# Kernel optimization log

Hardware: AMD Instinct MI355X
Metric: run time of the kernel (lower is better)

The kernel has to match this reference:

```python
import jax, jax.numpy as jnp
import numpy as np

HEADS = 4
DIM_HEAD = 64
MAP_SIZE = 16
SCALE = DIM_HEAD ** (-0.5)


def _split_heads(x):
    # torch rearrange 'b (dim_head heads) h w -> b heads (h w) dim_head'
    B, C, H, W = x.shape
    x = x.reshape(B, DIM_HEAD, HEADS, H * W)
    return jnp.transpose(x, (0, 2, 3, 1))  # [B, heads, N, dim_head]


def _merge_heads(x, H, W):
    # torch rearrange 'b heads (h w) dim_head -> b (dim_head heads) h w'
    B, h, N, d = x.shape
    return jnp.transpose(x, (0, 3, 1, 2)).reshape(B, d * h, H, W)


def setup_inputs() -> dict:
    key = jax.random.key(0)
    ks = jax.random.split(key, 6)
    feat = jax.random.normal(ks[0], (4, 256, 96, 96), jnp.float32)
    semantic_map = jax.random.normal(ks[1], (4, 256, 16, 16), jnp.float32)
    # 1x1 conv weights, shape [out_ch, in_ch]; scaled like fan-in init
    W_feat_qv = 0.05 * jax.random.normal(ks[2], (512, 256), jnp.float32)
    W_map_qv = 0.05 * jax.random.normal(ks[3], (512, 256), jnp.float32)
    W_feat_out = 0.05 * jax.random.normal(ks[4], (256, 256), jnp.float32)
    W_map_out = 0.05 * jax.random.normal(ks[5], (256, 256), jnp.float32)
    return {
        "feat": feat,
        "semantic_map": semantic_map,
        "W_feat_qv": W_feat_qv,
        "W_map_qv": W_map_qv,
        "W_feat_out": W_feat_out,
        "W_map_out": W_map_out,
    }


def reference(feat, semantic_map, W_feat_qv, W_map_qv, W_feat_out, W_map_out):
    B, C, H, W = feat.shape
    # 1x1 convs == per-pixel channel matmuls
    fqv = jnp.einsum("oc,bchw->bohw", W_feat_qv, feat)
    feat_q, feat_v = jnp.split(fqv, 2, axis=1)
    mqv = jnp.einsum("oc,bchw->bohw", W_map_qv, semantic_map)
    map_q, map_v = jnp.split(mqv, 2, axis=1)

    feat_q, feat_v = _split_heads(feat_q), _split_heads(feat_v)  # [B,h,N,d]
    map_q, map_v = _split_heads(map_q), _split_heads(map_v)      # [B,h,M,d]

    attn = jnp.einsum("bhid,bhjd->bhij", feat_q, map_q) * SCALE  # [B,h,N,M]
    feat_map_attn = jax.nn.softmax(attn, axis=-1)  # normalize over map tokens j
    map_feat_attn = jax.nn.softmax(attn, axis=-2)  # normalize over feat tokens i

    feat_o = jnp.einsum("bhij,bhjd->bhid", feat_map_attn, map_v)   # [B,h,N,d]
    map_o = jnp.einsum("bhji,bhjd->bhid", map_feat_attn, feat_v)   # [B,h,M,d]

    feat_o = _merge_heads(feat_o, H, W)
    map_o = _merge_heads(map_o, MAP_SIZE, MAP_SIZE)

    feat_out = jnp.einsum("oc,bchw->bohw", W_feat_out, feat_o)
    map_out = jnp.einsum("oc,bchw->bohw", W_map_out, map_o)
    return feat_out, map_out
```

## Files before the change

### kernel.cpp

```cpp
#include <hip/hip_runtime.h>
#include <stdint.h>

#define DI static __device__ __forceinline__

constexpr int NTOK = 9216;
constexpr float ATT_SCALE = 0.125f;

typedef short bf16x8 __attribute__((ext_vector_type(8)));
typedef float f32x4  __attribute__((ext_vector_type(4)));

DI f32x4 mfma16(bf16x8 a, bf16x8 b, f32x4 c) {
  return __builtin_amdgcn_mfma_f32_16x16x32_bf16(a, b, c, 0, 0, 0);
}

DI float lo2f(uint32_t u) { union { uint32_t i; float f; } v; v.i = u << 16; return v.f; }
DI float hi2f(uint32_t u) { union { uint32_t i; float f; } v; v.i = u & 0xffff0000u; return v.f; }
DI float b2f(uint16_t u) { union { uint32_t i; float f; } v; v.i = ((uint32_t)u) << 16; return v.f; }
DI uint16_t f2b(float f) {
  union { float f; uint32_t i; } v; v.f = f;
  uint32_t r = (v.i + 0x7fffu + ((v.i >> 16) & 1u)) >> 16;
  return (uint16_t)r;
}

template<int DT> DI float ld1(const void* p, size_t off) {
  if constexpr (DT) return b2f(((const uint16_t*)p)[off]);
  else              return ((const float*)p)[off];
}
template<int DT> DI void st1(void* p, size_t off, float v) {
  if constexpr (DT) ((uint16_t*)p)[off] = f2b(v);
  else              ((float*)p)[off] = v;
}
template<int DT> DI void load8(const void* p, size_t off, float* o) {
  if constexpr (DT) {
    const uint4 w = *(const uint4*)((const uint16_t*)p + off);
    o[0] = lo2f(w.x); o[1] = hi2f(w.x); o[2] = lo2f(w.y); o[3] = hi2f(w.y);
    o[4] = lo2f(w.z); o[5] = hi2f(w.z); o[6] = lo2f(w.w); o[7] = hi2f(w.w);
  } else {
    const float4 a = *(const float4*)((const float*)p + off);
    const float4 b = *(const float4*)((const float*)p + off + 4);
    o[0] = a.x; o[1] = a.y; o[2] = a.z; o[3] = a.w;
    o[4] = b.x; o[5] = b.y; o[6] = b.z; o[7] = b.w;
  }
}

__global__ void detect_dtype(const uint32_t* __restrict__ w, int* __restrict__ flag) {
  const int l = threadIdx.x;
  int cl = 0;
  #pragma unroll
  for (int i = 0; i < 4; ++i) {
    const float b = b2f((uint16_t)(w[l + i * 64] & 0xffffu));
    const float ab = fabsf(b);
    cl += (ab > 1e-4f && ab < 0.5f) ? 1 : 0;
  }
  cl += __shfl_xor(cl, 1);  cl += __shfl_xor(cl, 2);  cl += __shfl_xor(cl, 4);
  cl += __shfl_xor(cl, 8);  cl += __shfl_xor(cl, 16); cl += __shfl_xor(cl, 32);
  if (l == 0) flag[0] = (cl >= 128) ? 1 : 0;
}

template<int DT>
DI void prep_w_body(const void* __restrict__ Wfqv, const void* __restrict__ Wfo,
                    uint16_t* __restrict__ WqvP, uint16_t* __restrict__ WfoP)
{
  const int r = blockIdx.x, c = threadIdx.x;
  if (r < 512) {
    const int sel = r >> 8, within = r & 255;
    const int h = within >> 6, d = within & 63;
    const int src = sel * 256 + d * 4 + h;
    const int q = (c >> 3) & 3, j = c & 7;
    const int kp = (c & ~31) | (q << 3) | ((j + 2 * q) & 7);
    WqvP[(size_t)r * 256 + c] = f2b(ld1<DT>(Wfqv, (size_t)src * 256 + kp));
  } else {
    const int ro = r - 512;
    WfoP[(size_t)ro * 256 + c] =
        f2b(ld1<DT>(Wfo, (size_t)ro * 256 + (c & 63) * 4 + (c >> 6)));
  }
}
__global__ __launch_bounds__(256) void prep_w(
    const void* Wfqv, const void* Wfo, uint16_t* WqvP, uint16_t* WfoP,
    const int* __restrict__ flag)
{
  if (flag[0]) prep_w_body<1>(Wfqv, Wfo, WqvP, WfoP);
  else         prep_w_body<0>(Wfqv, Wfo, WqvP, WfoP);
}

constexpr int PB = 264;

template<int DT>
DI void gemm0_body(uint16_t* Bsh, const uint16_t* __restrict__ WqvP,
                   const void* __restrict__ X,
                   uint16_t* __restrict__ FQ, uint16_t* __restrict__ FVt)
{
  const int tid = threadIdx.x;
  const int w = tid >> 6, lane = tid & 63;
  const int l = lane & 15, quad = lane >> 4;
  const int n0 = blockIdx.x * 256;
  const int hh = blockIdx.y;
  const int bb = blockIdx.z;
  const size_t bh = (size_t)bb * 4 + hh;

  f32x4 acc[8][4];
  #pragma unroll
  for (int a = 0; a < 8; ++a)
    #pragma unroll
    for (int b = 0; b < 4; ++b) { acc[a][b].x = 0.f; acc[a][b].y = 0.f; acc[a][b].z = 0.f; acc[a][b].w = 0.f; }

  const int cst = tid >> 3;
  const int nst = (tid & 7) * 32;

  for (int ks = 0; ks < 8; ++ks) {
    {
      const size_t gbase = ((size_t)bb * 256 + ks * 32 + cst) * NTOK + n0 + nst;
      #pragma unroll
      for (int q = 0; q < 4; ++q) {
        if constexpr (DT) {
          *(uint4*)(Bsh + cst * PB + nst + q * 8) =
              *(const uint4*)((const uint16_t*)X + gbase + q * 8);
        } else {
          float xv[8];
          load8<0>(X, gbase + q * 8, xv);
          uint16_t pk[8];
          #pragma unroll
          for (int j = 0; j < 8; ++j) pk[j] = f2b(xv[j]);
          *(uint4*)(Bsh + cst * PB + nst + q * 8) = *(const uint4*)pk;
        }
      }
    }
    __syncthreads();
    bf16x8 af[8];
    #pragma unroll
    for (int mt = 0; mt < 8; ++mt) {
      const int arow = (mt >> 2) * 256 + hh * 64 + (mt & 3) * 16 + l;
      af[mt] = *(const bf16x8*)(WqvP + (size_t)arow * 256 + ks * 32 + quad * 8);
    }
    #pragma unroll
    for (int nt = 0; nt < 4; ++nt) {
      const int nl = w * 64 + nt * 16 + l;
      union { uint16_t h[8]; bf16x8 v; } bu;
      #pragma unroll
      for (int j = 0; j < 8; ++j)
        bu.h[j] = Bsh[(quad * 8 + ((j + 2 * quad) & 7)) * PB + nl];
      #pragma unroll
      for (int mt = 0; mt < 8; ++mt)
        acc[mt][nt] = mfma16(af[mt], bu.v, acc[mt][nt]);
    }
    __syncthreads();
  }
  #pragma unroll
  for (int mt = 0; mt < 8; ++mt)
    #pragma unroll
    for (int nt = 0; nt < 4; ++nt) {
      const int n = n0 + w * 64 + nt * 16 + l;
      if (mt < 4) {
        union { uint16_t h[4]; uint2 u; } pk;
        #pragma unroll
        for (int r = 0; r < 4; ++r) pk.h[r] = f2b(acc[mt][nt][r]);
        *(uint2*)(FQ + (bh * NTOK + n) * 64 + mt * 16 + quad * 4) = pk.u;
      } else {
        const int itile = n >> 5, io = n & 31;
        #pragma unroll
        for (int r = 0; r < 4; ++r)
          FVt[(((size_t)bh * 288 + itile) * 64 + (mt - 4) * 16 + quad * 4 + r) * 32 + io] =
              f2b(acc[mt][nt][r]);
      }
    }
}
__global__ __launch_bounds__(256) void gemm0_mfma(
    const uint16_t* WqvP, const void* X, uint16_t* FQ, uint16_t* FVt,
    const int* __restrict__ flag)
{
  __shared__ __align__(16) uint16_t Bsh[32 * PB];
  if (flag[0]) gemm0_body<1>(Bsh, WqvP, X, FQ, FVt);
  else         gemm0_body<0>(Bsh, WqvP, X, FQ, FVt);
}

template<int DT>
DI void gemm1_body(const uint16_t* __restrict__ WfoP, const uint16_t* __restrict__ FO,
                   void* __restrict__ out)
{
  const int tid = threadIdx.x;
  const int w = tid >> 6, lane = tid & 63;
  const int l = lane & 15, quad = lane >> 4;
  const int n0 = blockIdx.x * 256;
  const int o0 = blockIdx.y * 64;
  const int bb = blockIdx.z;

  f32x4 acc[4][4];
  #pragma unroll
  for (int a = 0; a < 4; ++a)
    #pragma unroll
    for (int b = 0; b < 4; ++b) { acc[a][b].x = 0.f; acc[a][b].y = 0.f; acc[a][b].z = 0.f; acc[a][b].w = 0.f; }

  for (int ks = 0; ks < 8; ++ks) {
    const int h2 = ks >> 1;
    const int doff = (ks & 1) * 32 + quad * 8;
    bf16x8 af[4];
    #pragma unroll
    for (int mt = 0; mt < 4; ++mt)
      af[mt] = *(const bf16x8*)(WfoP + (size_t)(o0 + mt * 16 + l) * 256 + ks * 32 + quad * 8);
    #pragma unroll
    for (int nt = 0; nt < 4; ++nt) {
      const int n = n0 + w * 64 + nt * 16 + l;
      const bf16x8 bv = *(const bf16x8*)(FO + ((size_t)(bb * 4 + h2) * NTOK + n) * 64 + doff);
      #pragma unroll
      for (int mt = 0; mt < 4; ++mt)
        acc[mt][nt] = mfma16(af[mt], bv, acc[mt][nt]);
    }
  }
  #pragma unroll
  for (int mt = 0; mt < 4; ++mt)
    #pragma unroll
    for (int nt = 0; nt < 4; ++nt) {
      const int n = n0 + w * 64 + nt * 16 + l;
      #pragma unroll
      for (int r = 0; r < 4; ++r)
        st1<DT>(out, ((size_t)bb * 256 + o0 + mt * 16 + quad * 4 + r) * NTOK + n,
                acc[mt][nt][r]);
    }
}
__global__ __launch_bounds__(256) void gemm1_mfma(
    const uint16_t* WfoP, const uint16_t* FO, void* out,
    const int* __restrict__ flag)
{
  if (flag[0]) gemm1_body<1>(WfoP, FO, out);
  else         gemm1_body<0>(WfoP, FO, out);
}

template<int DT>
DI void map_qv_body(const void* __restrict__ Wqv, const void* __restrict__ smap,
                    uint16_t* __restrict__ MQ, uint16_t* __restrict__ MVT)
{
  const int o = blockIdx.x, bb = blockIdx.y, m = threadIdx.x;
  float acc = 0.f;
  #pragma unroll 8
  for (int c = 0; c < 256; ++c)
    acc += ld1<DT>(Wqv, (size_t)o * 256 + c) *
           ld1<DT>(smap, (size_t)bb * 65536 + (size_t)c * 256 + m);
  const int oc = o & 255;
  const int h = oc & 3, d = oc >> 2;
  if (o < 256) MQ[(((size_t)bb * 4 + h) * 256 + m) * 64 + d] = f2b(acc);
  else         MVT[(((size_t)bb * 4 + h) * 64 + d) * 256 + m] = f2b(acc);
}
__global__ __launch_bounds__(256) void map_qv(
    const void* Wqv, const void* smap, uint16_t* MQ, uint16_t* MVT,
    const int* __restrict__ flag)
{
  if (flag[0]) map_qv_body<1>(Wqv, smap, MQ, MVT);
  else         map_qv_body<0>(Wqv, smap, MQ, MVT);
}

constexpr int PJ = 264;
constexpr int PI = 48;
constexpr int PO = 72;
constexpr int NGRP = 36;

__global__ __launch_bounds__(256, 3) void attn_mfma(
    const uint16_t* __restrict__ FQ, const uint16_t* __restrict__ FVt,
    const uint16_t* __restrict__ MQ, const uint16_t* __restrict__ MVT,
    uint16_t* __restrict__ FO, uint16_t* __restrict__ P)
{
  __shared__ __align__(16) uint16_t Esh[32 * PJ];
  __shared__ __align__(16) uint16_t ETsh[256 * PI];
  __shared__ __align__(16) uint16_t Osh[32 * PO];
  __shared__ float RS[4][32];
  const int tid = threadIdx.x;
  const int w = tid >> 6;
  const int lane = tid & 63;
  const int l = lane & 15, quad = lane >> 4;
  const int blk = blockIdx.x, bh = blockIdx.y;
  const uint16_t* FQh  = FQ  + (size_t)bh * NTOK * 64;
  const uint16_t* FVth = FVt + (size_t)bh * 288 * 64 * 32;
  const uint16_t* MQh  = MQ  + (size_t)bh * 256 * 64;
  const uint16_t* MVTh = MVT + (size_t)bh * 64 * 256;
  uint16_t* FOh = FO + (size_t)bh * NTOK * 64;

  f32x4 numacc[4][4];
  #pragma unroll
  for (int a = 0; a < 4; ++a)
    #pragma unroll
    for (int b = 0; b < 4; ++b) { numacc[a][b].x = 0.f; numacc[a][b].y = 0.f; numacc[a][b].z = 0.f; numacc[a][b].w = 0.f; }
  float csum[4] = {0.f, 0.f, 0.f, 0.f};

  for (int t = 0; t < 8; ++t) {
    const int it = blk * 8 + t;
    const int i0 = it * 32;

    bf16x8 qa[2][2];
    #pragma unroll
    for (int mt = 0; mt < 2; ++mt)
      #pragma unroll
      for (int kb = 0; kb < 2; ++kb)
        qa[mt][kb] = *(const bf16x8*)(FQh + (size_t)(i0 + mt * 16 + l) * 64 + kb * 32 + quad * 8);
    float rsum[2][4] = {{0.f,0.f,0.f,0.f},{0.f,0.f,0.f,0.f}};
    #pragma unroll
    for (int jt = 0; jt < 4; ++jt) {
      const int j0 = w * 64 + jt * 16;
      const bf16x8 kb0 = *(const bf16x8*)(MQh + (size_t)(j0 + l) * 64 + quad * 8);
      const bf16x8 kb1 = *(const bf16x8*)(MQh + (size_t)(j0 + l) * 64 + 32 + quad * 8);
      #pragma unroll
      for (int mt = 0; mt < 2; ++mt) {
        f32x4 acc = {0.f, 0.f, 0.f, 0.f};
        acc = mfma16(qa[mt][0], kb0, acc);
        acc = mfma16(qa[mt][1], kb1, acc);
        union { uint16_t h[4]; uint2 u; } pk;
        #pragma unroll
        for (int r = 0; r < 4; ++r) {
          const float e = __expf(acc[r] * ATT_SCALE);
          rsum[mt][r] += e;
          csum[jt] += e;
          pk.h[r] = f2b(e);
          Esh[(mt * 16 + quad * 4 + r) * PJ + j0 + l] = pk.h[r];
        }
        *(uint2*)(ETsh + (size_t)(j0 + l) * PI + mt * 16 + quad * 4) = pk.u;
      }
    }
    #pragma unroll
    for (int mt = 0; mt < 2; ++mt)
      #pragma unroll
      for (int r = 0; r < 4; ++r) {
        float v = rsum[mt][r];
        v += __shfl_xor(v, 1); v += __shfl_xor(v, 2);
        v += __shfl_xor(v, 4); v += __shfl_xor(v, 8);
        if (l == 0) RS[w][mt * 16 + quad * 4 + r] = v;
      }
    __syncthreads();

    {
      float rinv[2];
      #pragma unroll
      for (int nt = 0; nt < 2; ++nt) {
        const int i_ = nt * 16 + l;
        rinv[nt] = 1.f / (RS[0][i_] + RS[1][i_] + RS[2][i_] + RS[3][i_]);
      }
      f32x4 oacc[2];
      oacc[0].x=0.f;oacc[0].y=0.f;oacc[0].z=0.f;oacc[0].w=0.f;
      oacc[1]=oacc[0];
      #pragma unroll
      for (int ks = 0; ks < 8; ++ks) {
        const bf16x8 av = *(const bf16x8*)(MVTh + (size_t)(w * 16 + l) * 256 + ks * 32 + quad * 8);
        #pragma unroll
        for (int nt = 0; nt < 2; ++nt) {
          const bf16x8 bv = *(const bf16x8*)(Esh + (size_t)(nt * 16 + l) * PJ + ks * 32 + quad * 8);
          oacc[nt] = mfma16(av, bv, oacc[nt]);
        }
      }
      #pragma unroll
      for (int nt = 0; nt < 2; ++nt) {
        union { uint16_t h[4]; uint2 u; } pk;
        #pragma unroll
        for (int r = 0; r < 4; ++r) pk.h[r] = f2b(oacc[nt][r] * rinv[nt]);
        *(uint2*)(Osh + (nt * 16 + l) * PO + w * 16 + quad * 4) = pk.u;
      }
    }

    #pragma unroll
    for (int mt = 0; mt < 4; ++mt) {
      const bf16x8 av = *(const bf16x8*)(FVth + ((size_t)it * 64 + mt * 16 + l) * 32 + quad * 8);
      #pragma unroll
      for (int nt2 = 0; nt2 < 4; ++nt2) {
        const bf16x8 bv = *(const bf16x8*)(ETsh + (size_t)(w * 64 + nt2 * 16 + l) * PI + quad * 8);
        numacc[mt][nt2] = mfma16(av, bv, numacc[mt][nt2]);
      }
    }
    __syncthreads();

    {
      const int ti = tid >> 3, c = tid & 7;
      *(uint4*)(FOh + (size_t)(i0 + ti) * 64 + c * 8) =
          *(const uint4*)(Osh + ti * PO + c * 8);
    }
  }

  uint16_t* Pb = P + ((size_t)bh * NGRP + blk) * 65 * 256;
  #pragma unroll
  for (int mt = 0; mt < 4; ++mt)
    #pragma unroll
    for (int nt2 = 0; nt2 < 4; ++nt2)
      #pragma unroll
      for (int r = 0; r < 4; ++r)
        Pb[(mt * 16 + quad * 4 + r) * 256 + w * 64 + nt2 * 16 + l] =
            f2b(numacc[mt][nt2][r]);
  #pragma unroll
  for (int jt = 0; jt < 4; ++jt) {
    float v = csum[jt];
    v += __shfl_xor(v, 16); v += __shfl_xor(v, 32);
    if (quad == 0) Pb[64 * 256 + w * 64 + jt * 16 + l] = f2b(v);
  }
}

__global__ __launch_bounds__(256) void reduce_map(
    const uint16_t* __restrict__ P, uint16_t* __restrict__ MO)
{
  const int idx = blockIdx.x * 256 + threadIdx.x;
  const int bh = idx >> 14;
  const int d = (idx >> 8) & 63;
  const int j = idx & 255;
  const size_t base = (size_t)bh * NGRP * 65 * 256;
  float num = 0.f, cs = 0.f;
  #pragma unroll 6
  for (int g = 0; g < NGRP; ++g) {
    num += b2f(P[base + ((size_t)g * 65 + d) * 256 + j]);
    cs  += b2f(P[base + ((size_t)g * 65 + 64) * 256 + j]);
  }
  const float v = num / cs;
  const int b = bh >> 2, h = bh & 3;
  MO[((size_t)b * 256 + (d * 4 + h)) * 256 + j] = f2b(v);
}

template<int DT>
DI void map_out_body(const void* __restrict__ Wmo, const uint16_t* __restrict__ MO,
                     void* __restrict__ out)
{
  const int o = blockIdx.x, bb = blockIdx.y, m = threadIdx.x;
  float acc = 0.f;
  #pragma unroll 8
  for (int c = 0; c < 256; ++c)
    acc += ld1<DT>(Wmo, (size_t)o * 256 + c) *
           b2f(MO[((size_t)bb * 256 + c) * 256 + m]);
  const size_t MAP_OFS = (size_t)4 * 256 * NTOK;
  st1<DT>(out, MAP_OFS + ((size_t)bb * 256 + o) * 256 + m, acc);
}
__global__ __launch_bounds__(256) void map_out_k(
    const void* Wmo, const uint16_t* MO, void* out, const int* __restrict__ flag)
{
  if (flag[0]) map_out_body<1>(Wmo, MO, out);
  else         map_out_body<0>(Wmo, MO, out);
}

extern "C" void kernel_launch(void* const* d_in, const int* in_sizes, int n_in,
                              void* d_out, int out_size, void* d_ws, size_t ws_size,
                              hipStream_t stream) {
  (void)in_sizes; (void)n_in; (void)out_size; (void)ws_size;
  const void* feat = d_in[0];
  const void* smap = d_in[1];
  const void* Wfqv = d_in[2];
  const void* Wmqv = d_in[3];
  const void* Wfo  = d_in[4];
  const void* Wmo  = d_in[5];
  char* ws = (char*)d_ws;

  const size_t BIG = (size_t)16 * 64 * NTOK * 2;
  const size_t SML = (size_t)16 * 256 * 64 * 2;
  const size_t FQ_OFF  = 0;
  const size_t FVT_OFF = FQ_OFF + BIG;
  const size_t MQ_OFF  = FVT_OFF + BIG;
  const size_t MVT_OFF = MQ_OFF + SML;
  const size_t MO_OFF  = MVT_OFF + SML;
  const size_t WQP_OFF = MO_OFF + (size_t)4 * 256 * 256 * 2;
  const size_t WFP_OFF = WQP_OFF + (size_t)512 * 256 * 2;
  const size_t FLAG_OFF = WFP_OFF + (size_t)256 * 256 * 2;

  uint16_t* FQ   = (uint16_t*)(ws + FQ_OFF);
  uint16_t* FVt  = (uint16_t*)(ws + FVT_OFF);
  uint16_t* MQ   = (uint16_t*)(ws + MQ_OFF);
  uint16_t* MVT  = (uint16_t*)(ws + MVT_OFF);
  uint16_t* MO   = (uint16_t*)(ws + MO_OFF);
  uint16_t* WqvP = (uint16_t*)(ws + WQP_OFF);
  uint16_t* WfoP = (uint16_t*)(ws + WFP_OFF);
  int* FLAG   = (int*)(ws + FLAG_OFF);

  uint16_t* P = (uint16_t*)d_out;

  detect_dtype<<<dim3(1), dim3(64), 0, stream>>>((const uint32_t*)Wfqv, FLAG);
  prep_w<<<dim3(768), 256, 0, stream>>>(Wfqv, Wfo, WqvP, WfoP, FLAG);
  gemm0_mfma<<<dim3(36, 4, 4), 256, 0, stream>>>(WqvP, feat, FQ, FVt, FLAG);
  map_qv<<<dim3(512, 4), 256, 0, stream>>>(Wmqv, smap, MQ, MVT, FLAG);
  attn_mfma<<<dim3(NGRP, 16), 256, 0, stream>>>(FQ, FVt, MQ, MVT, FQ, P);
  reduce_map<<<dim3(1024), 256, 0, stream>>>(P, MO);
  gemm1_mfma<<<dim3(36, 4, 4), 256, 0, stream>>>(WfoP, FQ, d_out, FLAG);
  map_out_k<<<dim3(256, 4), 256, 0, stream>>>(Wmo, MO, d_out, FLAG);
}
```

Measured before the change: 314.6 us.

## Restructure QV projection tiling to load each feature tile once, prefetch attention operands

The QV projection GEMM now stages a 64-token by 256-channel feature tile into shared memory once, transposed so B fragments are contiguous vector loads. Each wave handles a different head, so the input is read once instead of once per head, and the per-k-step barriers disappear. The attention kernel prefetches the next tile's Q fragments and loads FV fragments at loop start to hide global latency, and several LDS padding constants change. The cost is scalar transposing LDS stores with possible bank conflicts, plus extra registers.

```diff
diff --git a/kernel.cpp b/kernel.cpp
--- a/kernel.cpp
+++ b/kernel.cpp
@@ -30,18 +30,6 @@
   if constexpr (DT) ((uint16_t*)p)[off] = f2b(v);
   else              ((float*)p)[off] = v;
 }
-template<int DT> DI void load8(const void* p, size_t off, float* o) {
-  if constexpr (DT) {
-    const uint4 w = *(const uint4*)((const uint16_t*)p + off);
-    o[0] = lo2f(w.x); o[1] = hi2f(w.x); o[2] = lo2f(w.y); o[3] = hi2f(w.y);
-    o[4] = lo2f(w.z); o[5] = hi2f(w.z); o[6] = lo2f(w.w); o[7] = hi2f(w.w);
-  } else {
-    const float4 a = *(const float4*)((const float*)p + off);
-    const float4 b = *(const float4*)((const float*)p + off + 4);
-    o[0] = a.x; o[1] = a.y; o[2] = a.z; o[3] = a.w;
-    o[4] = b.x; o[5] = b.y; o[6] = b.z; o[7] = b.w;
-  }
-}
 
 __global__ void detect_dtype(const uint32_t* __restrict__ w, int* __restrict__ flag) {
   const int l = threadIdx.x;
@@ -66,9 +54,7 @@
     const int sel = r >> 8, within = r & 255;
     const int h = within >> 6, d = within & 63;
     const int src = sel * 256 + d * 4 + h;
-    const int q = (c >> 3) & 3, j = c & 7;
-    const int kp = (c & ~31) | (q << 3) | ((j + 2 * q) & 7);
-    WqvP[(size_t)r * 256 + c] = f2b(ld1<DT>(Wfqv, (size_t)src * 256 + kp));
+    WqvP[(size_t)r * 256 + c] = f2b(ld1<DT>(Wfqv, (size_t)src * 256 + c));
   } else {
     const int ro = r - 512;
     WfoP[(size_t)ro * 256 + c] =
@@ -83,20 +69,48 @@
   else         prep_w_body<0>(Wfqv, Wfo, WqvP, WfoP);
 }
 
-constexpr int PB = 264;
+constexpr int P0 = 280;
 
 template<int DT>
-DI void gemm0_body(uint16_t* Bsh, const uint16_t* __restrict__ WqvP,
+DI void gemm0_body(uint16_t* Xs, const uint16_t* __restrict__ WqvP,
                    const void* __restrict__ X,
                    uint16_t* __restrict__ FQ, uint16_t* __restrict__ FVt)
 {
   const int tid = threadIdx.x;
   const int w = tid >> 6, lane = tid & 63;
   const int l = lane & 15, quad = lane >> 4;
-  const int n0 = blockIdx.x * 256;
-  const int hh = blockIdx.y;
-  const int bb = blockIdx.z;
-  const size_t bh = (size_t)bb * 4 + hh;
+  const int n0 = blockIdx.x * 64;
+  const int bb = blockIdx.y;
+  const size_t bh = (size_t)bb * 4 + w;
+
+  {
+    const int nh = (tid & 1) * 32;
+    #pragma unroll
+    for (int p = 0; p < 2; ++p) {
+      const int c = p * 128 + (tid >> 1);
+      const size_t g = ((size_t)bb * 256 + c) * NTOK + n0 + nh;
+      if constexpr (DT) {
+        #pragma unroll
+        for (int u = 0; u < 4; ++u) {
+          const uint4 v = *(const uint4*)((const uint16_t*)X + g + u * 8);
+          const uint16_t* pk = (const uint16_t*)&v;
+          #pragma unroll
+          for (int j = 0; j < 8; ++j)
+            Xs[(size_t)(nh + u * 8 + j) * P0 + c] = pk[j];
+        }
+      } else {
+        #pragma unroll
+        for (int u = 0; u < 8; ++u) {
+          const float4 v = *(const float4*)((const float*)X + g + u * 4);
+          Xs[(size_t)(nh + u * 4 + 0) * P0 + c] = f2b(v.x);
+          Xs[(size_t)(nh + u * 4 + 1) * P0 + c] = f2b(v.y);
+          Xs[(size_t)(nh + u * 4 + 2) * P0 + c] = f2b(v.z);
+          Xs[(size_t)(nh + u * 4 + 3) * P0 + c] = f2b(v.w);
+        }
+      }
+    }
+  }
+  __syncthreads();
 
   f32x4 acc[8][4];
   #pragma unroll
@@ -104,52 +118,26 @@
     #pragma unroll
     for (int b = 0; b < 4; ++b) { acc[a][b].x = 0.f; acc[a][b].y = 0.f; acc[a][b].z = 0.f; acc[a][b].w = 0.f; }
 
-  const int cst = tid >> 3;
-  const int nst = (tid & 7) * 32;
-
   for (int ks = 0; ks < 8; ++ks) {
-    {
-      const size_t gbase = ((size_t)bb * 256 + ks * 32 + cst) * NTOK + n0 + nst;
-      #pragma unroll
-      for (int q = 0; q < 4; ++q) {
-        if constexpr (DT) {
-          *(uint4*)(Bsh + cst * PB + nst + q * 8) =
-              *(const uint4*)((const uint16_t*)X + gbase + q * 8);
-        } else {
-          float xv[8];
-          load8<0>(X, gbase + q * 8, xv);
-          uint16_t pk[8];
-          #pragma unroll
-          for (int j = 0; j < 8; ++j) pk[j] = f2b(xv[j]);
-          *(uint4*)(Bsh + cst * PB + nst + q * 8) = *(const uint4*)pk;
-        }
-      }
-    }
-    __syncthreads();
     bf16x8 af[8];
     #pragma unroll
     for (int mt = 0; mt < 8; ++mt) {
-      const int arow = (mt >> 2) * 256 + hh * 64 + (mt & 3) * 16 + l;
+      const int arow = (mt >> 2) * 256 + w * 64 + (mt & 3) * 16 + l;
       af[mt] = *(const bf16x8*)(WqvP + (size_t)arow * 256 + ks * 32 + quad * 8);
     }
     #pragma unroll
     for (int nt = 0; nt < 4; ++nt) {
-      const int nl = w * 64 + nt * 16 + l;
-      union { uint16_t h[8]; bf16x8 v; } bu;
-      #pragma unroll
-      for (int j = 0; j < 8; ++j)
-        bu.h[j] = Bsh[(quad * 8 + ((j + 2 * quad) & 7)) * PB + nl];
+      const bf16x8 bv = *(const bf16x8*)(Xs + (size_t)(nt * 16 + l) * P0 + ks * 32 + quad * 8);
       #pragma unroll
       for (int mt = 0; mt < 8; ++mt)
-        acc[mt][nt] = mfma16(af[mt], bu.v, acc[mt][nt]);
-    }
-    __syncthreads();
+        acc[mt][nt] = mfma16(af[mt], bv, acc[mt][nt]);
+    }
   }
   #pragma unroll
   for (int mt = 0; mt < 8; ++mt)
     #pragma unroll
     for (int nt = 0; nt < 4; ++nt) {
-      const int n = n0 + w * 64 + nt * 16 + l;
+      const int n = n0 + nt * 16 + l;
       if (mt < 4) {
         union { uint16_t h[4]; uint2 u; } pk;
         #pragma unroll
@@ -168,9 +156,9 @@
     const uint16_t* WqvP, const void* X, uint16_t* FQ, uint16_t* FVt,
     const int* __restrict__ flag)
 {
-  __shared__ __align__(16) uint16_t Bsh[32 * PB];
-  if (flag[0]) gemm0_body<1>(Bsh, WqvP, X, FQ, FVt);
-  else         gemm0_body<0>(Bsh, WqvP, X, FQ, FVt);
+  __shared__ __align__(16) uint16_t Xs[64 * P0];
+  if (flag[0]) gemm0_body<1>(Xs, WqvP, X, FQ, FVt);
+  else         gemm0_body<0>(Xs, WqvP, X, FQ, FVt);
 }
 
 template<int DT>
@@ -248,8 +236,8 @@
   else         map_qv_body<0>(Wqv, smap, MQ, MVT);
 }
 
-constexpr int PJ = 264;
-constexpr int PI = 48;
+constexpr int PJ = 280;
+constexpr int PI = 40;
 constexpr int PO = 72;
 constexpr int NGRP = 36;
 
@@ -280,16 +268,36 @@
     for (int b = 0; b < 4; ++b) { numacc[a][b].x = 0.f; numacc[a][b].y = 0.f; numacc[a][b].z = 0.f; numacc[a][b].w = 0.f; }
   float csum[4] = {0.f, 0.f, 0.f, 0.f};
 
+  bf16x8 qa[2][2];
+  {
+    const int i0p = blk * 8 * 32;
+    #pragma unroll
+    for (int mt = 0; mt < 2; ++mt)
+      #pragma unroll
+      for (int kb = 0; kb < 2; ++kb)
+        qa[mt][kb] = *(const bf16x8*)(FQh + (size_t)(i0p + mt * 16 + l) * 64 + kb * 32 + quad * 8);
+  }
+
   for (int t = 0; t < 8; ++t) {
     const int it = blk * 8 + t;
     const int i0 = it * 32;
 
-    bf16x8 qa[2][2];
-    #pragma unroll
-    for (int mt = 0; mt < 2; ++mt)
-      #pragma unroll
-      for (int kb = 0; kb < 2; ++kb)
-        qa[mt][kb] = *(const bf16x8*)(FQh + (size_t)(i0 + mt * 16 + l) * 64 + kb * 32 + quad * 8);
+    bf16x8 av[4];
+    #pragma unroll
+    for (int mt = 0; mt < 4; ++mt)
+      av[mt] = *(const bf16x8*)(FVth + ((size_t)it * 64 + mt * 16 + l) * 32 + quad * 8);
+
+    bf16x8 qn[2][2];
+    {
+      const int itn = blk * 8 + ((t + 1) & 7);
+      const int i0n = itn * 32;
+      #pragma unroll
+      for (int mt = 0; mt < 2; ++mt)
+        #pragma unroll
+        for (int kb = 0; kb < 2; ++kb)
+          qn[mt][kb] = *(const bf16x8*)(FQh + (size_t)(i0n + mt * 16 + l) * 64 + kb * 32 + quad * 8);
+    }
+
     float rsum[2][4] = {{0.f,0.f,0.f,0.f},{0.f,0.f,0.f,0.f}};
     #pragma unroll
     for (int jt = 0; jt < 4; ++jt) {
@@ -336,11 +344,11 @@
       oacc[1]=oacc[0];
       #pragma unroll
       for (int ks = 0; ks < 8; ++ks) {
-        const bf16x8 av = *(const bf16x8*)(MVTh + (size_t)(w * 16 + l) * 256 + ks * 32 + quad * 8);
+        const bf16x8 avr = *(const bf16x8*)(MVTh + (size_t)(w * 16 + l) * 256 + ks * 32 + quad * 8);
         #pragma unroll
         for (int nt = 0; nt < 2; ++nt) {
           const bf16x8 bv = *(const bf16x8*)(Esh + (size_t)(nt * 16 + l) * PJ + ks * 32 + quad * 8);
-          oacc[nt] = mfma16(av, bv, oacc[nt]);
+          oacc[nt] = mfma16(avr, bv, oacc[nt]);
         }
       }
       #pragma unroll
@@ -354,11 +362,10 @@
 
     #pragma unroll
     for (int mt = 0; mt < 4; ++mt) {
-      const bf16x8 av = *(const bf16x8*)(FVth + ((size_t)it * 64 + mt * 16 + l) * 32 + quad * 8);
       #pragma unroll
       for (int nt2 = 0; nt2 < 4; ++nt2) {
         const bf16x8 bv = *(const bf16x8*)(ETsh + (size_t)(w * 64 + nt2 * 16 + l) * PI + quad * 8);
-        numacc[mt][nt2] = mfma16(av, bv, numacc[mt][nt2]);
+        numacc[mt][nt2] = mfma16(av[mt], bv, numacc[mt][nt2]);
       }
     }
     __syncthreads();
@@ -367,6 +374,12 @@
       const int ti = tid >> 3, c = tid & 7;
       *(uint4*)(FOh + (size_t)(i0 + ti) * 64 + c * 8) =
           *(const uint4*)(Osh + ti * PO + c * 8);
+    }
+
+    #pragma unroll
+    for (int mt = 0; mt < 2; ++mt) {
+      qa[mt][0] = qn[mt][0];
+      qa[mt][1] = qn[mt][1];
     }
   }
 
@@ -462,7 +475,7 @@
 
   detect_dtype<<<dim3(1), dim3(64), 0, stream>>>((const uint32_t*)Wfqv, FLAG);
   prep_w<<<dim3(768), 256, 0, stream>>>(Wfqv, Wfo, WqvP, WfoP, FLAG);
-  gemm0_mfma<<<dim3(36, 4, 4), 256, 0, stream>>>(WqvP, feat, FQ, FVt, FLAG);
+  gemm0_mfma<<<dim3(144, 4), 256, 0, stream>>>(WqvP, feat, FQ, FVt, FLAG);
   map_qv<<<dim3(512, 4), 256, 0, stream>>>(Wmqv, smap, MQ, MVT, FLAG);
   attn_mfma<<<dim3(NGRP, 16), 256, 0, stream>>>(FQ, FVt, MQ, MVT, FQ, P);
   reduce_map<<<dim3(1024), 256, 0, stream>>>(P, MO);
```

New measurement: 310.1 us. No clear change (-1.4%).
